# Optimization experiments

Measured on AMD Instinct MI355X. Metric: run time of the kernel, lower is better.

Reference implementation:

```python
import jax, jax.numpy as jnp
import numpy as np

B, LC, LQ, D = 64, 1024, 128, 128
NEG_BIG = 1.0e12


def _len_mask(seq_len, T):
    # seq_len: (B,1) int. Equivalent to 1 - cumsum(one_hot(L, T)): 1 for pos < L.
    pos = jnp.arange(T)  # (T,)
    return (pos[None, :] < seq_len).astype(jnp.float32)  # (B,T)


def setup_inputs() -> dict:
    key = jax.random.key(0)
    ks = jax.random.split(key, 7)
    return {
        "x_cont": jax.random.normal(ks[0], (B, LC, D), dtype=jnp.float32),
        "x_ques": jax.random.normal(ks[1], (B, LQ, D), dtype=jnp.float32),
        "W0": jax.random.normal(ks[2], (D, 1), dtype=jnp.float32) / np.sqrt(D),
        "W1": jax.random.normal(ks[3], (D, 1), dtype=jnp.float32) / np.sqrt(D),
        "W2": jax.random.normal(ks[4], (1, 1, D), dtype=jnp.float32) / np.sqrt(D),
        "cont_len": jax.random.randint(ks[5], (B, 1), 1, LC, dtype=jnp.int32),
        "ques_len": jax.random.randint(ks[6], (B, 1), 1, LQ, dtype=jnp.int32),
    }


def reference(x_cont, x_ques, W0, W1, W2, cont_len, ques_len):
    # Trilinear similarity: S[b,c,q] = x_cont@W0 + x_ques@W1 + (x_cont*W2) . x_ques
    s_cont = jnp.einsum('bcd,do->bco', x_cont, W0)            # (B,LC,1)
    s_ques = jnp.einsum('bqd,do->boq', x_ques, W1)            # (B,1,LQ)
    s_fuse = jnp.einsum('bcd,bqd->bcq', x_cont * W2, x_ques)  # (B,LC,LQ)
    S = s_cont + s_ques + s_fuse                               # (B,LC,LQ)

    mask_q = _len_mask(ques_len, LQ)  # (B,LQ)
    mask_c = _len_mask(cont_len, LC)  # (B,LC)

    # Softmax over query axis, masking invalid query positions (axis=-1)
    S_bar = jax.nn.softmax(S - (1.0 - mask_q)[:, None, :] * NEG_BIG, axis=-1)
    # Softmax over context axis, masking invalid context positions, then transpose
    S_T = jnp.swapaxes(
        jax.nn.softmax(S - (1.0 - mask_c)[:, :, None] * NEG_BIG, axis=1), 1, 2
    )  # (B,LQ,LC)

    c2q = jnp.einsum('bcq,bqd->bcd', S_bar, x_ques)             # (B,LC,D)
    q2c = jnp.einsum('bcq,bqk,bkd->bcd', S_bar, S_T, x_cont)    # (B,LC,D)

    result = jnp.concatenate(
        [x_cont, c2q, x_cont * c2q, x_cont * q2c], axis=-1
    )  # (B,LC,4D)
    return result, S_bar, S_T
```

## Files before the change

kernel.cpp:

```cpp
#include <hip/hip_runtime.h>

#define NB 64
#define LC 1024
#define LQ 128
#define DD 128
#define NEG_BIG 1.0e12f

typedef __attribute__((ext_vector_type(8))) short short8;
typedef __attribute__((ext_vector_type(4))) unsigned short ushort4v;
typedef __attribute__((ext_vector_type(4))) float floatx4;

__device__ __forceinline__ float wave_reduce_sum(float v) {
#pragma unroll
  for (int m = 32; m >= 1; m >>= 1) v += __shfl_xor(v, m, 64);
  return v;
}
__device__ __forceinline__ unsigned short f2bf(float f) {
  union { float f; unsigned int u; } v;
  v.f = f;
  const unsigned int r = v.u + 0x7FFFu + ((v.u >> 16) & 1u);
  return (unsigned short)(r >> 16);
}
__device__ __forceinline__ float bf2f(unsigned int u) {
  union { unsigned int u; float f; } v;
  v.u = u << 16;
  return v.f;
}

__global__ __launch_bounds__(256) void k_pre_c(
    const float* __restrict__ xc, const float* __restrict__ W0,
    unsigned short* __restrict__ xcT, float* __restrict__ a_cont) {
  __shared__ __align__(16) unsigned short tile[64 * 136];
  const int b = blockIdx.x >> 4;
  const int c0 = (blockIdx.x & 15) << 6;
  const int t = threadIdx.x;
  const int w = t >> 6, lane = t & 63;
  const float* src = xc + ((size_t)b * LC + c0) * DD;

#pragma unroll
  for (int i = 0; i < 8; ++i) {
    const int id = t + (i << 8);
    const int row = id >> 5, u = id & 31;
    const float4 v = *(const float4*)(src + (size_t)row * DD + (u << 2));
    ushort4v pk;
    pk[0] = f2bf(v.x); pk[1] = f2bf(v.y); pk[2] = f2bf(v.z); pk[3] = f2bf(v.w);
    *(ushort4v*)(tile + row * 136 + (u << 2)) = pk;
  }
  const float w0a = W0[lane << 1];
  const float w0b = W0[(lane << 1) + 1];
  __syncthreads();
#pragma unroll
  for (int r = 0; r < 16; ++r) {
    const int row = (w << 4) + r;
    const unsigned int pk = *(const unsigned int*)(tile + row * 136 + (lane << 1));
    float s = fmaf(bf2f(pk & 0xffffu), w0a, bf2f(pk >> 16) * w0b);
    s = wave_reduce_sum(s);
    if (lane == 0) a_cont[b * LC + c0 + row] = s;
  }
  const int d = t >> 1, ch = t & 1;
  short8 o[4];
#pragma unroll
  for (int j = 0; j < 32; ++j)
    ((unsigned short*)o)[j] = tile[(ch * 32 + j) * 136 + d];
  unsigned short* dp = xcT + ((size_t)b * DD + d) * LC + c0 + ch * 32;
#pragma unroll
  for (int j = 0; j < 4; ++j) *(short8*)(dp + (j << 3)) = o[j];
}

__global__ __launch_bounds__(256) void k_pre_q(
    const float* __restrict__ xq, const float* __restrict__ W1,
    unsigned short* __restrict__ xqT, float* __restrict__ a_ques) {
  __shared__ __align__(16) unsigned short tile[128 * 136];
  const int b = blockIdx.x;
  const int t = threadIdx.x;
  const int w = t >> 6, lane = t & 63;
  const float* src = xq + (size_t)b * LQ * DD;

#pragma unroll
  for (int i = 0; i < 16; ++i) {
    const int id = t + (i << 8);
    const int row = id >> 5, u = id & 31;
    const float4 v = *(const float4*)(src + (size_t)row * DD + (u << 2));
    ushort4v pk;
    pk[0] = f2bf(v.x); pk[1] = f2bf(v.y); pk[2] = f2bf(v.z); pk[3] = f2bf(v.w);
    *(ushort4v*)(tile + row * 136 + (u << 2)) = pk;
  }
  const float w1a = W1[lane << 1];
  const float w1b = W1[(lane << 1) + 1];
  __syncthreads();
#pragma unroll
  for (int r = 0; r < 32; ++r) {
    const int row = (w << 5) + r;
    const unsigned int pk = *(const unsigned int*)(tile + row * 136 + (lane << 1));
    float s = fmaf(bf2f(pk & 0xffffu), w1a, bf2f(pk >> 16) * w1b);
    s = wave_reduce_sum(s);
    if (lane == 0) a_ques[b * LQ + row] = s;
  }
  const int d = t >> 1, ch = t & 1;
  short8 o[8];
#pragma unroll
  for (int j = 0; j < 64; ++j)
    ((unsigned short*)o)[j] = tile[(ch * 64 + j) * 136 + d];
  unsigned short* dp = xqT + ((size_t)b * DD + d) * LQ + ch * 64;
#pragma unroll
  for (int j = 0; j < 8; ++j) *(short8*)(dp + (j << 3)) = o[j];
}

#define PADW 136

__global__ __launch_bounds__(512) void k_score(
    const float* __restrict__ xc, const float* __restrict__ xq,
    const float* __restrict__ w2, const float* __restrict__ a_cont,
    const float* __restrict__ a_ques, const int* __restrict__ qlen_p,
    const int* __restrict__ clen_p, float* __restrict__ out_sbar,
    unsigned short* __restrict__ Pb, float* __restrict__ colsum_part) {
  __shared__ __align__(16) unsigned short smem[2 * 128 * PADW];
  unsigned short* xcs = smem;
  unsigned short* xqs = smem + 128 * PADW;
  unsigned short* ptile = smem;

  const int b = blockIdx.x >> 3;
  const int ct = blockIdx.x & 7;
  const int c0 = ct << 7;
  const int t = threadIdx.x;
  const int w = t >> 6, lane = t & 63;
  const int frow = lane & 15;
  const int kb = lane >> 4;

  const float* xc_blk = xc + ((size_t)b * LC + c0) * DD;
  const float* xq_b = xq + (size_t)b * LQ * DD;

#pragma unroll
  for (int i = 0; i < 4; ++i) {
    const int id = t + (i << 9);
    const int row = id >> 4, u = id & 15;
    {
      const float4 v0 = *(const float4*)(xc_blk + (size_t)row * DD + (u << 3));
      const float4 v1 = *(const float4*)(xc_blk + (size_t)row * DD + (u << 3) + 4);
      short8 pk;
      pk[0] = (short)f2bf(v0.x); pk[1] = (short)f2bf(v0.y);
      pk[2] = (short)f2bf(v0.z); pk[3] = (short)f2bf(v0.w);
      pk[4] = (short)f2bf(v1.x); pk[5] = (short)f2bf(v1.y);
      pk[6] = (short)f2bf(v1.z); pk[7] = (short)f2bf(v1.w);
      *(short8*)(xcs + row * PADW + (u << 3)) = pk;
    }
    {
      const float4 v0 = *(const float4*)(xq_b + (size_t)row * DD + (u << 3));
      const float4 v1 = *(const float4*)(xq_b + (size_t)row * DD + (u << 3) + 4);
      const float4 w0 = *(const float4*)(w2 + (u << 3));
      const float4 w1 = *(const float4*)(w2 + (u << 3) + 4);
      short8 pk;
      pk[0] = (short)f2bf(v0.x * w0.x); pk[1] = (short)f2bf(v0.y * w0.y);
      pk[2] = (short)f2bf(v0.z * w0.z); pk[3] = (short)f2bf(v0.w * w0.w);
      pk[4] = (short)f2bf(v1.x * w1.x); pk[5] = (short)f2bf(v1.y * w1.y);
      pk[6] = (short)f2bf(v1.z * w1.z); pk[7] = (short)f2bf(v1.w * w1.w);
      *(short8*)(xqs + row * PADW + (u << 3)) = pk;
    }
  }

  const int qlen = qlen_p[b];
  const int clen = clen_p[b];
  float ac[4], aq[8];
#pragma unroll
  for (int reg = 0; reg < 4; ++reg)
    ac[reg] = a_cont[b * LC + c0 + w * 16 + kb * 4 + reg];
#pragma unroll
  for (int n = 0; n < 8; ++n) aq[n] = a_ques[b * LQ + n * 16 + frow];

  __syncthreads();

  floatx4 acc[8];
#pragma unroll
  for (int n = 0; n < 8; ++n) acc[n] = (floatx4){0.f, 0.f, 0.f, 0.f};
  const unsigned short* arow = xcs + (w * 16 + frow) * PADW + kb * 8;
  const unsigned short* brow = xqs + frow * PADW + kb * 8;
#pragma unroll
  for (int ks = 0; ks < 4; ++ks) {
    const short8 af = *(const short8*)(arow + ks * 32);
#pragma unroll
    for (int n = 0; n < 8; ++n) {
      const short8 bf = *(const short8*)(brow + n * 16 * PADW + ks * 32);
      acc[n] = __builtin_amdgcn_mfma_f32_16x16x32_bf16(af, bf, acc[n], 0, 0, 0);
    }
  }

  float raw[8][4];
#pragma unroll
  for (int n = 0; n < 8; ++n)
#pragma unroll
    for (int reg = 0; reg < 4; ++reg) raw[n][reg] = acc[n][reg] + ac[reg] + aq[n];

  float* sbar_row0 =
      out_sbar + ((size_t)b * LC + c0 + w * 16 + kb * 4) * LQ + frow;
#pragma unroll
  for (int reg = 0; reg < 4; ++reg) {
    float x[8];
    float m = -3.4e38f;
#pragma unroll
    for (int n = 0; n < 8; ++n) {
      x[n] = raw[n][reg] - ((n * 16 + frow) < qlen ? 0.f : NEG_BIG);
      m = fmaxf(m, x[n]);
    }
#pragma unroll
    for (int msk = 8; msk >= 1; msk >>= 1) m = fmaxf(m, __shfl_xor(m, msk, 64));
    float s = 0.f;
#pragma unroll
    for (int n = 0; n < 8; ++n) {
      x[n] = __expf(x[n] - m);
      s += x[n];
    }
#pragma unroll
    for (int msk = 8; msk >= 1; msk >>= 1) s += __shfl_xor(s, msk, 64);
    const float inv = 1.0f / s;
    float* o = sbar_row0 + (size_t)reg * LQ;
#pragma unroll
    for (int n = 0; n < 8; ++n) o[n * 16] = x[n] * inv;
  }

  const int cl0 = c0 + w * 16 + kb * 4;
#pragma unroll
  for (int reg = 0; reg < 4; ++reg) {
    const bool ok = (cl0 + reg) < clen;
#pragma unroll
    for (int n = 0; n < 8; ++n)
      raw[n][reg] = ok ? __expf(raw[n][reg]) : 0.f;
  }

  unsigned short* Pb_b = Pb + (size_t)b * LQ * LC;
  float* cs_blk = colsum_part + ((size_t)b * 8 + ct) * LQ;
#pragma unroll
  for (int p = 0; p < 4; ++p) {
    __syncthreads();
#pragma unroll
    for (int n2 = 0; n2 < 2; ++n2) {
#pragma unroll
      for (int reg = 0; reg < 4; ++reg)
        ptile[(n2 * 16 + frow) * 136 + (w * 16 + kb * 4 + reg)] =
            f2bf(raw[2 * p + n2][reg]);
    }
    __syncthreads();
    const int qrow = t >> 4;
    const int ch = t & 15;
    const short8 pv = *(const short8*)(ptile + qrow * 136 + (ch << 3));
    *(short8*)(Pb_b + (size_t)(p * 32 + qrow) * LC + c0 + (ch << 3)) = pv;
    float s = 0.f;
#pragma unroll
    for (int j = 0; j < 8; ++j) s += bf2f((unsigned short)pv[j]);
#pragma unroll
    for (int msk = 8; msk >= 1; msk >>= 1) s += __shfl_xor(s, msk, 64);
    if (ch == 0) cs_blk[p * 32 + qrow] = s;
  }
}

__global__ __launch_bounds__(256) void k_fuse(
    const unsigned short* __restrict__ Pb, const float* __restrict__ colsum_part,
    const unsigned short* __restrict__ xcT, float* __restrict__ st,
    unsigned short* __restrict__ AbT) {
  __shared__ __align__(16) unsigned short Ps[16 * 1032];
  __shared__ __align__(16) unsigned short bt[128 * 72];
  __shared__ unsigned short abt[128 * 20];
  __shared__ float inv_s[16];

  const int b = blockIdx.x >> 3;
  const int q0 = (blockIdx.x & 7) << 4;
  const int t = threadIdx.x;
  const int w = t >> 6, lane = t & 63;
  const int frow = lane & 15, kb = lane >> 4;

  const unsigned short* Pb_blk = Pb + ((size_t)b * LQ + q0) * LC;
  {
    const int row = t >> 4;
#pragma unroll
    for (int j = 0; j < 8; ++j) {
      const int cs = ((t & 15) << 3) + (j << 7);
      *(short8*)(Ps + row * 1032 + cs) =
          *(const short8*)(Pb_blk + (size_t)row * LC + cs);
    }
  }
  if (t < 16) {
    float s = 0.f;
#pragma unroll
    for (int j = 0; j < 8; ++j)
      s += colsum_part[((size_t)b * 8 + j) * LQ + q0 + t];
    inv_s[t] = 1.0f / s;
  }
  __syncthreads();

  {
    const int row = t >> 4;
    const float inv = inv_s[row];
    float* dst = st + ((size_t)b * LQ + q0 + row) * LC;
#pragma unroll
    for (int j = 0; j < 8; ++j) {
      const int cs = ((t & 15) << 3) + (j << 7);
      const short8 pv = *(const short8*)(Ps + row * 1032 + cs);
      float4 o0, o1;
      o0.x = bf2f((unsigned short)pv[0]) * inv;
      o0.y = bf2f((unsigned short)pv[1]) * inv;
      o0.z = bf2f((unsigned short)pv[2]) * inv;
      o0.w = bf2f((unsigned short)pv[3]) * inv;
      o1.x = bf2f((unsigned short)pv[4]) * inv;
      o1.y = bf2f((unsigned short)pv[5]) * inv;
      o1.z = bf2f((unsigned short)pv[6]) * inv;
      o1.w = bf2f((unsigned short)pv[7]) * inv;
      *(float4*)(dst + cs) = o0;
      *(float4*)(dst + cs + 4) = o1;
    }
  }

  const unsigned short* xcT_b = xcT + (size_t)b * DD * LC;
  floatx4 acc0 = (floatx4){0.f, 0.f, 0.f, 0.f};
  floatx4 acc1 = (floatx4){0.f, 0.f, 0.f, 0.f};
  for (int kc = 0; kc < 16; ++kc) {
    __syncthreads();
#pragma unroll
    for (int i = 0; i < 4; ++i) {
      const int id = t + (i << 8);
      const int row = id >> 3, u = id & 7;
      *(short8*)(bt + row * 72 + (u << 3)) =
          *(const short8*)(xcT_b + (size_t)row * LC + (kc << 6) + (u << 3));
    }
    __syncthreads();
#pragma unroll
    for (int ks = 0; ks < 2; ++ks) {
      const short8 af =
          *(const short8*)(Ps + frow * 1032 + (kc << 6) + ks * 32 + kb * 8);
      const short8 b0 =
          *(const short8*)(bt + ((w * 2 + 0) * 16 + frow) * 72 + ks * 32 + kb * 8);
      const short8 b1 =
          *(const short8*)(bt + ((w * 2 + 1) * 16 + frow) * 72 + ks * 32 + kb * 8);
      acc0 = __builtin_amdgcn_mfma_f32_16x16x32_bf16(af, b0, acc0, 0, 0, 0);
      acc1 = __builtin_amdgcn_mfma_f32_16x16x32_bf16(af, b1, acc1, 0, 0, 0);
    }
  }
  __syncthreads();
  const float i0 = inv_s[kb * 4 + 0], i1 = inv_s[kb * 4 + 1];
  const float i2 = inv_s[kb * 4 + 2], i3 = inv_s[kb * 4 + 3];
  {
    const int d0 = (w * 2 + 0) * 16 + frow;
    abt[d0 * 20 + kb * 4 + 0] = f2bf(acc0[0] * i0);
    abt[d0 * 20 + kb * 4 + 1] = f2bf(acc0[1] * i1);
    abt[d0 * 20 + kb * 4 + 2] = f2bf(acc0[2] * i2);
    abt[d0 * 20 + kb * 4 + 3] = f2bf(acc0[3] * i3);
    const int d1 = (w * 2 + 1) * 16 + frow;
    abt[d1 * 20 + kb * 4 + 0] = f2bf(acc1[0] * i0);
    abt[d1 * 20 + kb * 4 + 1] = f2bf(acc1[1] * i1);
    abt[d1 * 20 + kb * 4 + 2] = f2bf(acc1[2] * i2);
    abt[d1 * 20 + kb * 4 + 3] = f2bf(acc1[3] * i3);
  }
  __syncthreads();
  const int d = t >> 1, h = t & 1;
  short8 ov;
#pragma unroll
  for (int j = 0; j < 8; ++j)
    ((unsigned short*)&ov)[j] = abt[d * 20 + h * 8 + j];
  *(short8*)(AbT + ((size_t)b * DD + d) * LQ + q0 + h * 8) = ov;
}

__global__ __launch_bounds__(256) void k_out(
    const float* __restrict__ xc, const float* __restrict__ sbar,
    const unsigned short* __restrict__ xqT, const unsigned short* __restrict__ AbT,
    float* __restrict__ out) {
  __shared__ __align__(16) float stg[2 * 32 * 132];
  unsigned short* sbs = (unsigned short*)stg;

  const int b = blockIdx.x >> 4;
  const int c0 = (blockIdx.x & 15) << 6;
  const int t = threadIdx.x;
  const int w = t >> 6, lane = t & 63;
  const int frow = lane & 15, kb = lane >> 4;

  const float* sb_blk = sbar + ((size_t)b * LC + c0) * LQ;
#pragma unroll
  for (int i = 0; i < 8; ++i) {
    const int id = t + (i << 8);
    const int row = id >> 5, u = id & 31;
    const float4 v = *(const float4*)(sb_blk + (size_t)row * LQ + (u << 2));
    ushort4v pk;
    pk[0] = f2bf(v.x); pk[1] = f2bf(v.y); pk[2] = f2bf(v.z); pk[3] = f2bf(v.w);
    *(ushort4v*)(sbs + row * 136 + (u << 2)) = pk;
  }

  const unsigned short* xqT_b = xqT + (size_t)b * DD * LQ;
  const unsigned short* AbT_b = AbT + (size_t)b * DD * LQ;
  short8 bq[2][4], ba[2][4];
#pragma unroll
  for (int nt = 0; nt < 2; ++nt) {
    const int d = (w << 5) + (nt << 4) + frow;
#pragma unroll
    for (int ks = 0; ks < 4; ++ks) {
      bq[nt][ks] = *(const short8*)(xqT_b + (size_t)d * LQ + ks * 32 + kb * 8);
      ba[nt][ks] = *(const short8*)(AbT_b + (size_t)d * LQ + ks * 32 + kb * 8);
    }
  }
  __syncthreads();

  floatx4 accq[4][2], acca[4][2];
#pragma unroll
  for (int mt = 0; mt < 4; ++mt)
#pragma unroll
    for (int nt = 0; nt < 2; ++nt) {
      accq[mt][nt] = (floatx4){0.f, 0.f, 0.f, 0.f};
      acca[mt][nt] = (floatx4){0.f, 0.f, 0.f, 0.f};
    }
#pragma unroll
  for (int mt = 0; mt < 4; ++mt) {
#pragma unroll
    for (int ks = 0; ks < 4; ++ks) {
      const short8 af =
          *(const short8*)(sbs + ((mt << 4) + frow) * 136 + ks * 32 + kb * 8);
#pragma unroll
      for (int nt = 0; nt < 2; ++nt) {
        accq[mt][nt] =
            __builtin_amdgcn_mfma_f32_16x16x32_bf16(af, bq[nt][ks], accq[mt][nt], 0, 0, 0);
        acca[mt][nt] =
            __builtin_amdgcn_mfma_f32_16x16x32_bf16(af, ba[nt][ks], acca[mt][nt], 0, 0, 0);
      }
    }
  }

  float* out_b = out + ((size_t)b * LC + c0) * (4 * DD);
  const float* xc_blk = xc + ((size_t)b * LC + c0) * DD;

#pragma unroll
  for (int p = 0; p < 2; ++p) {
    __syncthreads();
#pragma unroll
    for (int mh = 0; mh < 2; ++mh) {
      const int mt = 2 * p + mh;
#pragma unroll
      for (int nt = 0; nt < 2; ++nt) {
        const int d = (w << 5) + (nt << 4) + frow;
        const int cl = (mh << 4) + (kb << 2);
#pragma unroll
        for (int reg = 0; reg < 4; ++reg) {
          stg[(cl + reg) * 132 + d] = accq[mt][nt][reg];
          stg[32 * 132 + (cl + reg) * 132 + d] = acca[mt][nt][reg];
        }
      }
    }
    __syncthreads();
    const int g = lane >> 4;
    const int d0 = (lane & 15) << 3;
#pragma unroll
    for (int j = 0; j < 8; ++j) {
      const int rl = (w << 3) + j;
      const int c = (p << 5) + rl;
      const float4 xv0 = *(const float4*)(xc_blk + (size_t)c * DD + d0);
      const float4 xv1 = *(const float4*)(xc_blk + (size_t)c * DD + d0 + 4);
      const float4 cq0 = *(const float4*)(stg + rl * 132 + d0);
      const float4 cq1 = *(const float4*)(stg + rl * 132 + d0 + 4);
      const float4 qc0 = *(const float4*)(stg + 32 * 132 + rl * 132 + d0);
      const float4 qc1 = *(const float4*)(stg + 32 * 132 + rl * 132 + d0 + 4);
      float4 o0, o1;
      if (g == 0) { o0 = xv0; o1 = xv1; }
      else if (g == 1) { o0 = cq0; o1 = cq1; }
      else if (g == 2) {
        o0 = make_float4(xv0.x * cq0.x, xv0.y * cq0.y, xv0.z * cq0.z, xv0.w * cq0.w);
        o1 = make_float4(xv1.x * cq1.x, xv1.y * cq1.y, xv1.z * cq1.z, xv1.w * cq1.w);
      } else {
        o0 = make_float4(xv0.x * qc0.x, xv0.y * qc0.y, xv0.z * qc0.z, xv0.w * qc0.w);
        o1 = make_float4(xv1.x * qc1.x, xv1.y * qc1.y, xv1.z * qc1.z, xv1.w * qc1.w);
      }
      float* o = out_b + (size_t)c * (4 * DD) + (g << 7) + d0;
      *(float4*)(o) = o0;
      *(float4*)(o + 4) = o1;
    }
  }
}

extern "C" void kernel_launch(void* const* d_in, const int* in_sizes, int n_in,
                              void* d_out, int out_size, void* d_ws, size_t ws_size,
                              hipStream_t stream) {
  const float* xc = (const float*)d_in[0];
  const float* xq = (const float*)d_in[1];
  const float* W0 = (const float*)d_in[2];
  const float* W1 = (const float*)d_in[3];
  const float* W2 = (const float*)d_in[4];
  const int* clen = (const int*)d_in[5];
  const int* qlen = (const int*)d_in[6];

  float* out = (float*)d_out;
  float* out_sbar = out + (size_t)NB * LC * 4 * DD;
  float* out_st = out_sbar + (size_t)NB * LC * LQ;

  float* a_cont = (float*)d_ws;
  float* a_ques = a_cont + NB * LC;
  float* colsum_part = a_ques + NB * LQ;
  unsigned short* xcT = (unsigned short*)(colsum_part + NB * 8 * LQ);
  unsigned short* xqT = xcT + (size_t)NB * LC * DD;
  unsigned short* AbT = xqT + (size_t)NB * LQ * DD;
  unsigned short* Pb = AbT + (size_t)NB * LQ * DD;

  k_pre_c<<<NB * 16, 256, 0, stream>>>(xc, W0, xcT, a_cont);
  k_pre_q<<<NB, 256, 0, stream>>>(xq, W1, xqT, a_ques);
  k_score<<<NB * 8, 512, 0, stream>>>(xc, xq, W2, a_cont, a_ques, qlen, clen,
                                      out_sbar, Pb, colsum_part);
  k_fuse<<<NB * 8, 256, 0, stream>>>(Pb, colsum_part, xcT, out_st, AbT);
  k_out<<<NB * 16, 256, 0, stream>>>(xc, out_sbar, xqT, AbT, out);
}
```

Measured before the change: 124.9 us.

## Fold context preprocessing into score kernel and pass bf16 S_bar to output kernel

Removes the separate k_pre_c launch: k_score now computes the x_cont·W0 term in shared memory and writes the bf16 transposed x_cont itself, since it already loads that tile. k_score also writes a bf16 copy of S_bar to workspace, and k_out reads MFMA A fragments straight from it instead of re-reading the fp32 S_bar and converting it. This cuts one launch and a re-read of x_cont and fp32 S_bar, at the cost of extra work, shared-memory staging passes and barriers in k_score, plus an extra bf16 write.

```diff
diff --git a/kernel.cpp b/kernel.cpp
--- a/kernel.cpp
+++ b/kernel.cpp
@@ -25,46 +25,6 @@
   union { unsigned int u; float f; } v;
   v.u = u << 16;
   return v.f;
-}
-
-__global__ __launch_bounds__(256) void k_pre_c(
-    const float* __restrict__ xc, const float* __restrict__ W0,
-    unsigned short* __restrict__ xcT, float* __restrict__ a_cont) {
-  __shared__ __align__(16) unsigned short tile[64 * 136];
-  const int b = blockIdx.x >> 4;
-  const int c0 = (blockIdx.x & 15) << 6;
-  const int t = threadIdx.x;
-  const int w = t >> 6, lane = t & 63;
-  const float* src = xc + ((size_t)b * LC + c0) * DD;
-
-#pragma unroll
-  for (int i = 0; i < 8; ++i) {
-    const int id = t + (i << 8);
-    const int row = id >> 5, u = id & 31;
-    const float4 v = *(const float4*)(src + (size_t)row * DD + (u << 2));
-    ushort4v pk;
-    pk[0] = f2bf(v.x); pk[1] = f2bf(v.y); pk[2] = f2bf(v.z); pk[3] = f2bf(v.w);
-    *(ushort4v*)(tile + row * 136 + (u << 2)) = pk;
-  }
-  const float w0a = W0[lane << 1];
-  const float w0b = W0[(lane << 1) + 1];
-  __syncthreads();
-#pragma unroll
-  for (int r = 0; r < 16; ++r) {
-    const int row = (w << 4) + r;
-    const unsigned int pk = *(const unsigned int*)(tile + row * 136 + (lane << 1));
-    float s = fmaf(bf2f(pk & 0xffffu), w0a, bf2f(pk >> 16) * w0b);
-    s = wave_reduce_sum(s);
-    if (lane == 0) a_cont[b * LC + c0 + row] = s;
-  }
-  const int d = t >> 1, ch = t & 1;
-  short8 o[4];
-#pragma unroll
-  for (int j = 0; j < 32; ++j)
-    ((unsigned short*)o)[j] = tile[(ch * 32 + j) * 136 + d];
-  unsigned short* dp = xcT + ((size_t)b * DD + d) * LC + c0 + ch * 32;
-#pragma unroll
-  for (int j = 0; j < 4; ++j) *(short8*)(dp + (j << 3)) = o[j];
 }
 
 __global__ __launch_bounds__(256) void k_pre_q(
@@ -110,14 +70,16 @@
 
 __global__ __launch_bounds__(512) void k_score(
     const float* __restrict__ xc, const float* __restrict__ xq,
-    const float* __restrict__ w2, const float* __restrict__ a_cont,
+    const float* __restrict__ w2, const float* __restrict__ W0,
     const float* __restrict__ a_ques, const int* __restrict__ qlen_p,
     const int* __restrict__ clen_p, float* __restrict__ out_sbar,
-    unsigned short* __restrict__ Pb, float* __restrict__ colsum_part) {
+    unsigned short* __restrict__ Pb, float* __restrict__ colsum_part,
+    unsigned short* __restrict__ xcT, unsigned short* __restrict__ sbarb) {
   __shared__ __align__(16) unsigned short smem[2 * 128 * PADW];
+  __shared__ float a_cont_s[128];
   unsigned short* xcs = smem;
   unsigned short* xqs = smem + 128 * PADW;
-  unsigned short* ptile = smem;
+  unsigned short* ptile = smem + 128 * PADW;
 
   const int b = blockIdx.x >> 3;
   const int ct = blockIdx.x & 7;
@@ -130,10 +92,15 @@
   const float* xc_blk = xc + ((size_t)b * LC + c0) * DD;
   const float* xq_b = xq + (size_t)b * LQ * DD;
 
+  const int u = t & 15;
+  const float4 w0a = *(const float4*)(W0 + (u << 3));
+  const float4 w0b = *(const float4*)(W0 + (u << 3) + 4);
+  const float4 w2a = *(const float4*)(w2 + (u << 3));
+  const float4 w2b = *(const float4*)(w2 + (u << 3) + 4);
+
 #pragma unroll
   for (int i = 0; i < 4; ++i) {
-    const int id = t + (i << 9);
-    const int row = id >> 4, u = id & 15;
+    const int row = (t >> 4) + (i << 5);
     {
       const float4 v0 = *(const float4*)(xc_blk + (size_t)row * DD + (u << 3));
       const float4 v1 = *(const float4*)(xc_blk + (size_t)row * DD + (u << 3) + 4);
@@ -143,31 +110,36 @@
       pk[4] = (short)f2bf(v1.x); pk[5] = (short)f2bf(v1.y);
       pk[6] = (short)f2bf(v1.z); pk[7] = (short)f2bf(v1.w);
       *(short8*)(xcs + row * PADW + (u << 3)) = pk;
+      float pd = v0.x * w0a.x + v0.y * w0a.y + v0.z * w0a.z + v0.w * w0a.w +
+                 v1.x * w0b.x + v1.y * w0b.y + v1.z * w0b.z + v1.w * w0b.w;
+#pragma unroll
+      for (int msk = 8; msk >= 1; msk >>= 1) pd += __shfl_xor(pd, msk, 64);
+      if ((lane & 15) == 0) a_cont_s[row] = pd;
     }
     {
       const float4 v0 = *(const float4*)(xq_b + (size_t)row * DD + (u << 3));
       const float4 v1 = *(const float4*)(xq_b + (size_t)row * DD + (u << 3) + 4);
-      const float4 w0 = *(const float4*)(w2 + (u << 3));
-      const float4 w1 = *(const float4*)(w2 + (u << 3) + 4);
       short8 pk;
-      pk[0] = (short)f2bf(v0.x * w0.x); pk[1] = (short)f2bf(v0.y * w0.y);
-      pk[2] = (short)f2bf(v0.z * w0.z); pk[3] = (short)f2bf(v0.w * w0.w);
-      pk[4] = (short)f2bf(v1.x * w1.x); pk[5] = (short)f2bf(v1.y * w1.y);
-      pk[6] = (short)f2bf(v1.z * w1.z); pk[7] = (short)f2bf(v1.w * w1.w);
+      pk[0] = (short)f2bf(v0.x * w2a.x); pk[1] = (short)f2bf(v0.y * w2a.y);
+      pk[2] = (short)f2bf(v0.z * w2a.z); pk[3] = (short)f2bf(v0.w * w2a.w);
+      pk[4] = (short)f2bf(v1.x * w2b.x); pk[5] = (short)f2bf(v1.y * w2b.y);
+      pk[6] = (short)f2bf(v1.z * w2b.z); pk[7] = (short)f2bf(v1.w * w2b.w);
       *(short8*)(xqs + row * PADW + (u << 3)) = pk;
     }
   }
 
   const int qlen = qlen_p[b];
   const int clen = clen_p[b];
-  float ac[4], aq[8];
+  float aq[8];
+#pragma unroll
+  for (int n = 0; n < 8; ++n) aq[n] = a_ques[b * LQ + n * 16 + frow];
+
+  __syncthreads();
+
+  float ac[4];
 #pragma unroll
   for (int reg = 0; reg < 4; ++reg)
-    ac[reg] = a_cont[b * LC + c0 + w * 16 + kb * 4 + reg];
-#pragma unroll
-  for (int n = 0; n < 8; ++n) aq[n] = a_ques[b * LQ + n * 16 + frow];
-
-  __syncthreads();
+    ac[reg] = a_cont_s[w * 16 + kb * 4 + reg];
 
   floatx4 acc[8];
 #pragma unroll
@@ -184,12 +156,26 @@
     }
   }
 
+  {
+    const int d = t & 127;
+    const int half = t >> 7;
+    __align__(16) unsigned short tmp[32];
+#pragma unroll
+    for (int j = 0; j < 32; ++j)
+      tmp[j] = xcs[((half << 5) + j) * PADW + d];
+    unsigned short* dp = xcT + ((size_t)b * DD + d) * LC + c0 + (half << 5);
+#pragma unroll
+    for (int j = 0; j < 4; ++j)
+      *(short8*)(dp + (j << 3)) = *(const short8*)(tmp + (j << 3));
+  }
+
   float raw[8][4];
 #pragma unroll
   for (int n = 0; n < 8; ++n)
 #pragma unroll
     for (int reg = 0; reg < 4; ++reg) raw[n][reg] = acc[n][reg] + ac[reg] + aq[n];
 
+  float mreg[4], invreg[4];
   float* sbar_row0 =
       out_sbar + ((size_t)b * LC + c0 + w * 16 + kb * 4) * LQ + frow;
 #pragma unroll
@@ -215,6 +201,30 @@
     float* o = sbar_row0 + (size_t)reg * LQ;
 #pragma unroll
     for (int n = 0; n < 8; ++n) o[n * 16] = x[n] * inv;
+    mreg[reg] = m;
+    invreg[reg] = inv;
+  }
+
+  unsigned short* sb_out = sbarb + ((size_t)b * LC + c0) * LQ;
+#pragma unroll
+  for (int p = 0; p < 4; ++p) {
+    __syncthreads();
+    if ((w >> 1) == p) {
+      const int crow = ((w & 1) << 4) + (kb << 2);
+#pragma unroll
+      for (int reg = 0; reg < 4; ++reg) {
+        const float m = mreg[reg], inv = invreg[reg];
+#pragma unroll
+        for (int n = 0; n < 8; ++n) {
+          const float xv = raw[n][reg] - ((n * 16 + frow) < qlen ? 0.f : NEG_BIG);
+          ptile[(crow + reg) * 136 + (n << 4) + frow] = f2bf(__expf(xv - m) * inv);
+        }
+      }
+    }
+    __syncthreads();
+    const int row = t >> 4, ch = t & 15;
+    *(short8*)(sb_out + (size_t)((p << 5) + row) * LQ + (ch << 3)) =
+        *(const short8*)(ptile + row * 136 + (ch << 3));
   }
 
   const int cl0 = c0 + w * 16 + kb * 4;
@@ -358,11 +368,10 @@
 }
 
 __global__ __launch_bounds__(256) void k_out(
-    const float* __restrict__ xc, const float* __restrict__ sbar,
+    const float* __restrict__ xc, const unsigned short* __restrict__ sbarb,
     const unsigned short* __restrict__ xqT, const unsigned short* __restrict__ AbT,
     float* __restrict__ out) {
   __shared__ __align__(16) float stg[2 * 32 * 132];
-  unsigned short* sbs = (unsigned short*)stg;
 
   const int b = blockIdx.x >> 4;
   const int c0 = (blockIdx.x & 15) << 6;
@@ -370,17 +379,7 @@
   const int w = t >> 6, lane = t & 63;
   const int frow = lane & 15, kb = lane >> 4;
 
-  const float* sb_blk = sbar + ((size_t)b * LC + c0) * LQ;
-#pragma unroll
-  for (int i = 0; i < 8; ++i) {
-    const int id = t + (i << 8);
-    const int row = id >> 5, u = id & 31;
-    const float4 v = *(const float4*)(sb_blk + (size_t)row * LQ + (u << 2));
-    ushort4v pk;
-    pk[0] = f2bf(v.x); pk[1] = f2bf(v.y); pk[2] = f2bf(v.z); pk[3] = f2bf(v.w);
-    *(ushort4v*)(sbs + row * 136 + (u << 2)) = pk;
-  }
-
+  const unsigned short* sb_blk = sbarb + ((size_t)b * LC + c0) * LQ;
   const unsigned short* xqT_b = xqT + (size_t)b * DD * LQ;
   const unsigned short* AbT_b = AbT + (size_t)b * DD * LQ;
   short8 bq[2][4], ba[2][4];
@@ -393,7 +392,6 @@
       ba[nt][ks] = *(const short8*)(AbT_b + (size_t)d * LQ + ks * 32 + kb * 8);
     }
   }
-  __syncthreads();
 
   floatx4 accq[4][2], acca[4][2];
 #pragma unroll
@@ -407,8 +405,8 @@
   for (int mt = 0; mt < 4; ++mt) {
 #pragma unroll
     for (int ks = 0; ks < 4; ++ks) {
-      const short8 af =
-          *(const short8*)(sbs + ((mt << 4) + frow) * 136 + ks * 32 + kb * 8);
+      const short8 af = *(const short8*)(
+          sb_blk + (size_t)((mt << 4) + frow) * LQ + ks * 32 + kb * 8);
 #pragma unroll
       for (int nt = 0; nt < 2; ++nt) {
         accq[mt][nt] =
@@ -484,18 +482,17 @@
   float* out_sbar = out + (size_t)NB * LC * 4 * DD;
   float* out_st = out_sbar + (size_t)NB * LC * LQ;
 
-  float* a_cont = (float*)d_ws;
-  float* a_ques = a_cont + NB * LC;
+  float* a_ques = (float*)d_ws;
   float* colsum_part = a_ques + NB * LQ;
   unsigned short* xcT = (unsigned short*)(colsum_part + NB * 8 * LQ);
   unsigned short* xqT = xcT + (size_t)NB * LC * DD;
   unsigned short* AbT = xqT + (size_t)NB * LQ * DD;
   unsigned short* Pb = AbT + (size_t)NB * LQ * DD;
-
-  k_pre_c<<<NB * 16, 256, 0, stream>>>(xc, W0, xcT, a_cont);
+  unsigned short* sbarb = Pb + (size_t)NB * LQ * LC;
+
   k_pre_q<<<NB, 256, 0, stream>>>(xq, W1, xqT, a_ques);
-  k_score<<<NB * 8, 512, 0, stream>>>(xc, xq, W2, a_cont, a_ques, qlen, clen,
-                                      out_sbar, Pb, colsum_part);
+  k_score<<<NB * 8, 512, 0, stream>>>(xc, xq, W2, W0, a_ques, qlen, clen,
+                                      out_sbar, Pb, colsum_part, xcT, sbarb);
   k_fuse<<<NB * 8, 256, 0, stream>>>(Pb, colsum_part, xcT, out_st, AbT);
-  k_out<<<NB * 16, 256, 0, stream>>>(xc, out_sbar, xqT, AbT, out);
-}
+  k_out<<<NB * 16, 256, 0, stream>>>(xc, sbarb, xqT, AbT, out);
+}
```

Result: faster. 121.4 us (-2.8%).
